# Optimization experiments

Measured on AMD Instinct MI355X. Metric: run time of the kernel, lower is better.

The kernel has to match this reference:

```python
import jax, jax.numpy as jnp
import numpy as np

NUM_HEADS = 16
NUM_KV_HEADS = 4
HEAD_DIM = 128
HALF_DIM = HEAD_DIM // 2
LAMBDA_INIT = 0.8
LAMBDA_MIN = 0.0
LAMBDA_MAX = 1.0
CAUSAL = True
NORMALIZE_DIFF = True
NEG = -1.0e9


def setup_inputs() -> dict:
    key = jax.random.key(0)
    k1, k2, k3 = jax.random.split(key, 3)
    B, Sq, Sk = 1, 2048, 2048
    query = jax.random.normal(k1, (B, NUM_HEADS, Sq, HEAD_DIM), dtype=jnp.float32)
    key_t = jax.random.normal(k2, (B, NUM_KV_HEADS, Sk, HEAD_DIM), dtype=jnp.float32)
    value = jax.random.normal(k3, (B, NUM_KV_HEADS, Sk, HEAD_DIM), dtype=jnp.float32)
    return {"query": query, "key": key_t, "value": value}


def reference(query, key, value):
    scale = 1.0 / (HALF_DIM ** 0.5)
    lam = jnp.clip(jnp.float32(LAMBDA_INIT), LAMBDA_MIN, LAMBDA_MAX)
    # GQA: repeat KV heads to match query heads
    rep = NUM_HEADS // NUM_KV_HEADS
    k = jnp.repeat(key, rep, axis=1)    # [b,h,k,d]
    v = jnp.repeat(value, rep, axis=1)  # [b,h,k,d]
    q1, q2 = query[..., :HALF_DIM], query[..., HALF_DIM:]
    k1, k2 = k[..., :HALF_DIM], k[..., HALF_DIM:]
    scores1 = jnp.einsum('bhqd,bhkd->bhqk', q1, k1) * scale
    scores2 = jnp.einsum('bhqd,bhkd->bhqk', q2, k2) * scale
    if CAUSAL:
        Sq, Sk = query.shape[2], k.shape[2]
        mask = jnp.tril(jnp.ones((Sq, Sk), dtype=jnp.float32))  # lower-triangular causal
        scores1 = scores1 * mask + (1.0 - mask) * NEG
        scores2 = scores2 * mask + (1.0 - mask) * NEG
    attn1 = jax.nn.softmax(scores1, axis=-1)
    attn2 = jax.nn.softmax(scores2, axis=-1)
    diff_attn = attn1 - lam * attn2
    out = jnp.einsum('bhqk,bhkd->bhqd', diff_attn, v)
    if NORMALIZE_DIFF:
        out = out * (1.0 - LAMBDA_INIT)
    return out
```

## Files before the change

kernel.cpp:

```cpp
#include <hip/hip_runtime.h>

#define NUM_HEADS 16
#define HEAD_DIM  128
#define SEQ       2048

typedef __attribute__((ext_vector_type(8))) unsigned short us8;
typedef __attribute__((ext_vector_type(8))) __bf16 bf16x8;
typedef __attribute__((ext_vector_type(4))) float f32x4;
typedef __attribute__((ext_vector_type(16))) float f32x16;
typedef __attribute__((ext_vector_type(4))) unsigned u32x4;

static __device__ inline unsigned short f2bf(float x) {
    union { float f; unsigned u; } v; v.f = x;
    unsigned r = v.u + 0x7FFFu + ((v.u >> 16) & 1u);
    return (unsigned short)(r >> 16);
}
static __device__ inline float bf2f(unsigned short h) {
    union { float f; unsigned u; } v; v.u = ((unsigned)h) << 16;
    return v.f;
}
static __device__ inline unsigned pk2bf(float a, float b) {
    return (unsigned)f2bf(a) | ((unsigned)f2bf(b) << 16);
}
static __device__ inline float fast_exp2(float x) {
#if __has_builtin(__builtin_amdgcn_exp2f)
    return __builtin_amdgcn_exp2f(x);
#else
    return exp2f(x);
#endif
}
static __device__ inline f32x16 mfma32(us8 a, us8 b, f32x16 c) {
    return __builtin_amdgcn_mfma_f32_32x32x16_bf16(
        __builtin_bit_cast(bf16x8, a), __builtin_bit_cast(bf16x8, b), c, 0, 0, 0);
}

__global__ __launch_bounds__(256)
void prep_kv(const float* __restrict__ K, const float* __restrict__ V,
             unsigned short* __restrict__ Kbf, unsigned short* __restrict__ Vtb)
{
    const int bx = (int)blockIdx.x, t = (int)threadIdx.x;
    __shared__ __align__(16) float Ls[64][130];
    if (bx < 512) {
        const size_t base = ((size_t)bx * 256 + t) * 8;
        float x[8];
        *(float4*)&x[0] = *(const float4*)(K + base);
        *(float4*)&x[4] = *(const float4*)(K + base + 4);
        u32x4 pk;
        #pragma unroll
        for (int j = 0; j < 4; ++j) pk[j] = pk2bf(x[2*j], x[2*j+1]);
        *(us8*)(Kbf + base) = __builtin_bit_cast(us8, pk);
    } else {
        const int b2 = bx - 512, kvh = b2 >> 5, tile = b2 & 31;
        const float* vb = V + ((size_t)kvh * SEQ + tile * 64) * HEAD_DIM;
        #pragma unroll
        for (int i = 0; i < 8; ++i) {
            const int idx = t + i * 256;
            const int r = idx >> 5, c4 = idx & 31;
            *(float4*)&Ls[r][c4 * 4] = *(const float4*)(vb + (size_t)r * HEAD_DIM + c4 * 4);
        }
        __syncthreads();
        const int d = t & 127, kh = t >> 7;
        unsigned pk[16];
        #pragma unroll
        for (int j = 0; j < 16; ++j)
            pk[j] = pk2bf(Ls[kh * 32 + 2*j][d], Ls[kh * 32 + 2*j + 1][d]);
        unsigned short* dst = Vtb + ((size_t)(kvh * 32 + tile) * 128 + d) * 64 + kh * 32;
        #pragma unroll
        for (int blk = 0; blk < 4; ++blk)
            *(us8*)(dst + blk * 8) = *(us8*)&pk[blk * 4];
    }
}

#define KB0 0
#define KB1 16384
#define VB0 32768
#define VB1 49152

__global__ __launch_bounds__(256, 2)
void diff_attn_mfma6(const float* __restrict__ Q,
                     const unsigned short* __restrict__ Kbf,
                     const unsigned short* __restrict__ Vtb,
                     float* __restrict__ Out)
{
    __shared__ __align__(16) unsigned char smem[65536];
    __shared__ float rsb[2][2][32];

    const int t   = (int)threadIdx.x;
    const int wv  = t >> 6;
    const int ln  = t & 63;
    const int mat = wv >> 1;
    const int kh  = wv & 1;
    const int q   = ln & 31;
    const int H   = ln >> 5;

    const int bx   = (int)blockIdx.x;
    const int h    = bx & 15;
    const int idx  = bx >> 4;
    const int qtA  = idx, qtB = 63 - idx;
    const int nktA = (qtA >> 1) + 1;
    const int kvh  = h >> 2;

    const unsigned short* Kt0 = Kbf + (size_t)kvh * SEQ * HEAD_DIM;
    const unsigned short* Vt0 = Vtb + (size_t)kvh * 32 * 128 * 64;

    const float qscale = 0.125f * 1.44269504088896340736f;

    us8 qhi[4], qlo[4];
    auto loadQ = [&](int q0c) {
        const float* qr = Q + ((size_t)h * SEQ + q0c + q) * HEAD_DIM + mat * 64;
        #pragma unroll
        for (int ds = 0; ds < 4; ++ds) {
            const int d0 = ds * 16 + H * 8;
            float x[8];
            *(float4*)&x[0] = *(const float4*)(qr + d0);
            *(float4*)&x[4] = *(const float4*)(qr + d0 + 4);
            us8 hi8, lo8;
            #pragma unroll
            for (int j = 0; j < 8; ++j) {
                float xs = x[j] * qscale;
                unsigned short hb = f2bf(xs);
                hi8[j] = hb;
                lo8[j] = f2bf(xs - bf2f(hb));
            }
            qhi[ds] = hi8; qlo[ds] = lo8;
        }
    };

    f32x16 o[4];
    f32x4 rsv;
    #pragma unroll
    for (int i = 0; i < 4; ++i) o[i] = (f32x16)0.f;
    rsv = (f32x4)0.f;

    auto issue = [&](int kt, int par) {
        unsigned char* kb = smem + (par ? KB1 : KB0);
        unsigned char* vb = smem + (par ? VB1 : VB0);
        #pragma unroll
        for (int i = 0; i < 4; ++i) {
            const int L = i * 256 + t;
            const int r = L >> 4, g = (L & 15) ^ (r & 15);
            const unsigned short* gp = Kt0 + (size_t)(kt * 64 + r) * 128 + g * 8;
            __builtin_amdgcn_global_load_lds(
                (const __attribute__((address_space(1))) unsigned*)gp,
                (__attribute__((address_space(3))) unsigned*)(kb + (size_t)(i * 256 + wv * 64) * 16),
                16, 0, 0);
        }
        #pragma unroll
        for (int i = 0; i < 4; ++i) {
            const int L = i * 256 + t;
            const int r = L >> 3, g = (L & 7) ^ (r & 7);
            const unsigned short* gp = Vt0 + (size_t)(kt * 128 + r) * 64 + g * 8;
            __builtin_amdgcn_global_load_lds(
                (const __attribute__((address_space(1))) unsigned*)gp,
                (__attribute__((address_space(3))) unsigned*)(vb + (size_t)(i * 256 + wv * 64) * 16),
                16, 0, 0);
        }
    };

    auto epilogue = [&](int q0c, int epar) {
        __syncthreads();
        float rsc = (rsv[0] + rsv[1]) + (rsv[2] + rsv[3]);
        rsc += __shfl_xor(rsc, 32, 64);
        if (ln < 32) rsb[mat][kh][ln] = rsc;
        float* cbK = (float*)(smem + (epar ? KB1 : KB0));
        float* cbV = (float*)(smem + (epar ? VB1 : VB0));
        float* cbM = mat ? cbV : cbK;
        if (kh == 1) {
            #pragma unroll
            for (int db = 0; db < 4; ++db)
                #pragma unroll
                for (int i = 0; i < 4; ++i) {
                    f32x4 v = { o[db][i*4+0], o[db][i*4+1], o[db][i*4+2], o[db][i*4+3] };
                    *(f32x4*)(cbM + q * 128 + ((((db<<3)+(i<<1)+H) ^ q) << 2)) = v;
                }
        }
        __syncthreads();
        if (kh == 0) {
            const float l = rsb[mat][0][q] + rsb[mat][1][q];
            const float a = mat ? (0.16f / l) : (0.2f / l);
            #pragma unroll
            for (int db = 0; db < 4; ++db)
                #pragma unroll
                for (int i = 0; i < 4; ++i) {
                    f32x4 v = *(f32x4*)(cbM + q * 128 + ((((db<<3)+(i<<1)+H) ^ q) << 2));
                    #pragma unroll
                    for (int jj = 0; jj < 4; ++jj)
                        o[db][i*4+jj] = (o[db][i*4+jj] + v[jj]) * a;
                }
            if (mat == 1) {
                #pragma unroll
                for (int db = 0; db < 4; ++db)
                    #pragma unroll
                    for (int i = 0; i < 4; ++i) {
                        f32x4 v = { o[db][i*4+0], o[db][i*4+1], o[db][i*4+2], o[db][i*4+3] };
                        *(f32x4*)(cbV + q * 128 + ((((db<<3)+(i<<1)+H) ^ q) << 2)) = v;
                    }
            }
        }
        __syncthreads();
        if (wv == 0) {
            float* ob = Out + ((size_t)h * SEQ + q0c + q) * HEAD_DIM;
            #pragma unroll
            for (int db = 0; db < 4; ++db)
                #pragma unroll
                for (int i = 0; i < 4; ++i) {
                    f32x4 v = *(f32x4*)(cbV + q * 128 + ((((db<<3)+(i<<1)+H) ^ q) << 2));
                    float4 r;
                    r.x = o[db][i*4+0] - v[0];
                    r.y = o[db][i*4+1] - v[1];
                    r.z = o[db][i*4+2] - v[2];
                    r.w = o[db][i*4+3] - v[3];
                    *(float4*)(ob + db * 32 + 8 * i + 4 * H) = r;
                }
        }
    };

    int q0 = qtA * 32, qt_cur = qtA;
    loadQ(q0);
    issue(0, 0);

    for (int j = 0; j < 33; ++j) {
        if (j == nktA) {
            epilogue(q0, (nktA - 1) & 1);
            q0 = qtB * 32; qt_cur = qtB;
            loadQ(q0);
            #pragma unroll
            for (int i = 0; i < 4; ++i) o[i] = (f32x16)0.f;
            rsv = (f32x4)0.f;
        }
        const int cur = j & 1;
        __syncthreads();
        if (j + 1 < 33) issue((j + 1 < nktA) ? j + 1 : j + 1 - nktA, cur ^ 1);

        const int kt = (j < nktA) ? j : j - nktA;
        const unsigned char* kbase = smem + (cur ? KB1 : KB0);
        const unsigned char* vbase = smem + (cur ? VB1 : VB0);
        const bool diag  = (j == nktA - 1) || (j == 32);
        const int  qpar  = qt_cur & 1;
        const bool skipw = diag && (qpar == 0) && (kh == 1);
        const bool triw  = diag && (kh == qpar);

        if (!skipw) {
            f32x16 s = (f32x16)0.f;
            const int krow = kh * 32 + q;
            #pragma unroll
            for (int ds = 0; ds < 4; ++ds) {
                us8 ak = *(const us8*)(kbase +
                          ((krow << 4) + ((mat * 8 + ds * 2 + H) ^ (krow & 15))) * 16);
                s = mfma32(ak, qhi[ds], s);
                s = mfma32(ak, qlo[ds], s);
            }
            unsigned c[16];
            if (triw) {
                const int kg0 = kt * 64 + kh * 32 + 4 * H;
                const int qg  = q0 + q;
                #pragma unroll
                for (int r = 0; r < 16; ++r) {
                    const int kg = kg0 + (r & 3) + ((r >> 2) << 3);
                    float e = (kg <= qg) ? fast_exp2(s[r]) : 0.f;
                    c[r] = __builtin_bit_cast(unsigned, e) & 0xffff0000u;
                    rsv[r & 3] += __builtin_bit_cast(float, c[r]);
                }
            } else {
                #pragma unroll
                for (int r = 0; r < 16; ++r) {
                    float e = fast_exp2(s[r]);
                    c[r] = __builtin_bit_cast(unsigned, e) & 0xffff0000u;
                    rsv[r & 3] += __builtin_bit_cast(float, c[r]);
                }
            }
            #pragma unroll
            for (int ks = 0; ks < 2; ++ks) {
                const unsigned pA = (c[8*ks+0] >> 16) | c[8*ks+1];
                const unsigned pB = (c[8*ks+2] >> 16) | c[8*ks+3];
                const unsigned pC = (c[8*ks+4] >> 16) | c[8*ks+5];
                const unsigned pD = (c[8*ks+6] >> 16) | c[8*ks+7];
                const unsigned x1 = H ? pA : pC;
                const unsigned x2 = H ? pB : pD;
                const unsigned t1 = (unsigned)__shfl_xor((int)x1, 32, 64);
                const unsigned t2 = (unsigned)__shfl_xor((int)x2, 32, 64);
                u32x4 bw;
                bw[0] = H ? t1 : pA;
                bw[1] = H ? t2 : pB;
                bw[2] = H ? pC : t1;
                bw[3] = H ? pD : t2;
                const us8 bp = __builtin_bit_cast(us8, bw);
                const int gb = kh * 4 + ks * 2 + H;
                #pragma unroll
                for (int db = 0; db < 4; ++db) {
                    const int r = db * 32 + q;
                    us8 av = *(const us8*)(vbase + ((r << 3) + (gb ^ (r & 7))) * 16);
                    o[db] = mfma32(av, bp, o[db]);
                }
            }
        }
    }

    epilogue(q0, 0);
}

extern "C" void kernel_launch(void* const* d_in, const int* in_sizes, int n_in,
                              void* d_out, int out_size, void* d_ws, size_t ws_size,
                              hipStream_t stream) {
    const float* Q = (const float*)d_in[0];
    const float* K = (const float*)d_in[1];
    const float* V = (const float*)d_in[2];
    float* Out = (float*)d_out;

    unsigned short* Kbf = (unsigned short*)d_ws;
    unsigned short* Vtb = Kbf + (size_t)4 * SEQ * HEAD_DIM;

    prep_kv<<<640, 256, 0, stream>>>(K, V, Kbf, Vtb);
    diff_attn_mfma6<<<512, 256, 0, stream>>>(Q, Kbf, Vtb, Out);
}
```

Before: 125.3 us.

## Pre-swizzle K/V into MFMA fragment layout and load directly to registers

The prep kernel now writes K and V in bf16 already arranged in per-lane MFMA operand fragment order. The attention kernel then loads each wave's operands straight from global memory into registers instead of staging tiles in LDS with global_load_lds and barriers. The next K tile is prefetched one iteration ahead in registers, and the per-iteration __syncthreads goes away. The cost is that each wave fetches its own fragments with no reuse through LDS, which relies on L2 and L1 caching and exposes more load latency. Register pressure also rises from holding 16 extra us8 fragments.

```diff
diff --git a/kernel.cpp b/kernel.cpp
--- a/kernel.cpp
+++ b/kernel.cpp
@@ -3,6 +3,7 @@
 #define NUM_HEADS 16
 #define HEAD_DIM  128
 #define SEQ       2048
+#define KT_STRIDE 8192
 
 typedef __attribute__((ext_vector_type(8))) unsigned short us8;
 typedef __attribute__((ext_vector_type(8))) __bf16 bf16x8;
@@ -35,54 +36,62 @@
 }
 
 __global__ __launch_bounds__(256)
-void prep_kv(const float* __restrict__ K, const float* __restrict__ V,
-             unsigned short* __restrict__ Kbf, unsigned short* __restrict__ Vtb)
+void prep_frag(const float* __restrict__ K, const float* __restrict__ V,
+               unsigned short* __restrict__ KF, unsigned short* __restrict__ VF)
 {
-    const int bx = (int)blockIdx.x, t = (int)threadIdx.x;
-    __shared__ __align__(16) float Ls[64][130];
-    if (bx < 512) {
-        const size_t base = ((size_t)bx * 256 + t) * 8;
-        float x[8];
-        *(float4*)&x[0] = *(const float4*)(K + base);
-        *(float4*)&x[4] = *(const float4*)(K + base + 4);
-        u32x4 pk;
+    const int bx  = (int)blockIdx.x, t = (int)threadIdx.x;
+    const int which = bx & 1, kt = (bx >> 1) & 31, kvh = bx >> 6;
+    __shared__ __align__(16) float Ls[64][132];
+
+    const float* src = (which ? V : K) + ((size_t)kvh * SEQ + kt * 64) * HEAD_DIM;
+    #pragma unroll
+    for (int i = 0; i < 8; ++i) {
+        const int idx = t + i * 256;
+        const int r = idx >> 5, c4 = idx & 31;
+        *(float4*)&Ls[r][c4 * 4] = *(const float4*)(src + (size_t)r * HEAD_DIM + c4 * 4);
+    }
+    __syncthreads();
+
+    if (!which) {
         #pragma unroll
-        for (int j = 0; j < 4; ++j) pk[j] = pk2bf(x[2*j], x[2*j+1]);
-        *(us8*)(Kbf + base) = __builtin_bit_cast(us8, pk);
+        for (int i = 0; i < 4; ++i) {
+            const int c = t + i * 256;
+            const int lane = c & 63, ds = (c >> 6) & 3, mat = (c >> 8) & 1, kh = c >> 9;
+            const int H = lane >> 5;
+            const int row = kh * 32 + (lane & 31);
+            const int dim = mat * 64 + ds * 16 + H * 8;
+            u32x4 pk;
+            #pragma unroll
+            for (int jj = 0; jj < 4; ++jj)
+                pk[jj] = pk2bf(Ls[row][dim + 2*jj], Ls[row][dim + 2*jj + 1]);
+            *(us8*)(KF + ((size_t)(kvh * 32 + kt) * 16 + kh * 8 + mat * 4 + ds) * 512 + lane * 8)
+                = __builtin_bit_cast(us8, pk);
+        }
     } else {
-        const int b2 = bx - 512, kvh = b2 >> 5, tile = b2 & 31;
-        const float* vb = V + ((size_t)kvh * SEQ + tile * 64) * HEAD_DIM;
         #pragma unroll
-        for (int i = 0; i < 8; ++i) {
-            const int idx = t + i * 256;
-            const int r = idx >> 5, c4 = idx & 31;
-            *(float4*)&Ls[r][c4 * 4] = *(const float4*)(vb + (size_t)r * HEAD_DIM + c4 * 4);
-        }
-        __syncthreads();
-        const int d = t & 127, kh = t >> 7;
-        unsigned pk[16];
-        #pragma unroll
-        for (int j = 0; j < 16; ++j)
-            pk[j] = pk2bf(Ls[kh * 32 + 2*j][d], Ls[kh * 32 + 2*j + 1][d]);
-        unsigned short* dst = Vtb + ((size_t)(kvh * 32 + tile) * 128 + d) * 64 + kh * 32;
-        #pragma unroll
-        for (int blk = 0; blk < 4; ++blk)
-            *(us8*)(dst + blk * 8) = *(us8*)&pk[blk * 4];
+        for (int i = 0; i < 4; ++i) {
+            const int c = t + i * 256;
+            const int lane = c & 63, db = (c >> 6) & 3, ks = (c >> 8) & 1, kh = c >> 9;
+            const int H = lane >> 5;
+            const int s0 = kh * 32 + ks * 16 + H * 8;
+            const int d  = db * 32 + (lane & 31);
+            u32x4 pk;
+            #pragma unroll
+            for (int jj = 0; jj < 4; ++jj)
+                pk[jj] = pk2bf(Ls[s0 + 2*jj][d], Ls[s0 + 2*jj + 1][d]);
+            *(us8*)(VF + ((size_t)(kvh * 32 + kt) * 16 + kh * 8 + ks * 4 + db) * 512 + lane * 8)
+                = __builtin_bit_cast(us8, pk);
+        }
     }
 }
 
-#define KB0 0
-#define KB1 16384
-#define VB0 32768
-#define VB1 49152
-
 __global__ __launch_bounds__(256, 2)
-void diff_attn_mfma6(const float* __restrict__ Q,
-                     const unsigned short* __restrict__ Kbf,
-                     const unsigned short* __restrict__ Vtb,
+void diff_attn_mfma7(const float* __restrict__ Q,
+                     const unsigned short* __restrict__ KF,
+                     const unsigned short* __restrict__ VF,
                      float* __restrict__ Out)
 {
-    __shared__ __align__(16) unsigned char smem[65536];
+    __shared__ float cb[2][32][136];
     __shared__ float rsb[2][2][32];
 
     const int t   = (int)threadIdx.x;
@@ -100,8 +109,8 @@
     const int nktA = (qtA >> 1) + 1;
     const int kvh  = h >> 2;
 
-    const unsigned short* Kt0 = Kbf + (size_t)kvh * SEQ * HEAD_DIM;
-    const unsigned short* Vt0 = Vtb + (size_t)kvh * 32 * 128 * 64;
+    const unsigned short* kfb = KF + ((size_t)kvh * 32 * 16 + kh * 8 + mat * 4) * 512 + ln * 8;
+    const unsigned short* vfb = VF + ((size_t)kvh * 32 * 16 + kh * 8) * 512 + ln * 8;
 
     const float qscale = 0.125f * 1.44269504088896340736f;
 
@@ -127,51 +136,22 @@
     };
 
     f32x16 o[4];
-    f32x4 rsv;
+    f32x4  rsv = (f32x4)0.f;
     #pragma unroll
     for (int i = 0; i < 4; ++i) o[i] = (f32x16)0.f;
-    rsv = (f32x4)0.f;
-
-    auto issue = [&](int kt, int par) {
-        unsigned char* kb = smem + (par ? KB1 : KB0);
-        unsigned char* vb = smem + (par ? VB1 : VB0);
-        #pragma unroll
-        for (int i = 0; i < 4; ++i) {
-            const int L = i * 256 + t;
-            const int r = L >> 4, g = (L & 15) ^ (r & 15);
-            const unsigned short* gp = Kt0 + (size_t)(kt * 64 + r) * 128 + g * 8;
-            __builtin_amdgcn_global_load_lds(
-                (const __attribute__((address_space(1))) unsigned*)gp,
-                (__attribute__((address_space(3))) unsigned*)(kb + (size_t)(i * 256 + wv * 64) * 16),
-                16, 0, 0);
-        }
-        #pragma unroll
-        for (int i = 0; i < 4; ++i) {
-            const int L = i * 256 + t;
-            const int r = L >> 3, g = (L & 7) ^ (r & 7);
-            const unsigned short* gp = Vt0 + (size_t)(kt * 128 + r) * 64 + g * 8;
-            __builtin_amdgcn_global_load_lds(
-                (const __attribute__((address_space(1))) unsigned*)gp,
-                (__attribute__((address_space(3))) unsigned*)(vb + (size_t)(i * 256 + wv * 64) * 16),
-                16, 0, 0);
-        }
-    };
-
-    auto epilogue = [&](int q0c, int epar) {
+
+    auto epilogue = [&](int q0c) {
         __syncthreads();
         float rsc = (rsv[0] + rsv[1]) + (rsv[2] + rsv[3]);
         rsc += __shfl_xor(rsc, 32, 64);
         if (ln < 32) rsb[mat][kh][ln] = rsc;
-        float* cbK = (float*)(smem + (epar ? KB1 : KB0));
-        float* cbV = (float*)(smem + (epar ? VB1 : VB0));
-        float* cbM = mat ? cbV : cbK;
         if (kh == 1) {
             #pragma unroll
             for (int db = 0; db < 4; ++db)
                 #pragma unroll
                 for (int i = 0; i < 4; ++i) {
-                    f32x4 v = { o[db][i*4+0], o[db][i*4+1], o[db][i*4+2], o[db][i*4+3] };
-                    *(f32x4*)(cbM + q * 128 + ((((db<<3)+(i<<1)+H) ^ q) << 2)) = v;
+                    float4 v = { o[db][i*4+0], o[db][i*4+1], o[db][i*4+2], o[db][i*4+3] };
+                    *(float4*)&cb[mat][q][db * 32 + 8 * i + 4 * H] = v;
                 }
         }
         __syncthreads();
@@ -182,18 +162,19 @@
             for (int db = 0; db < 4; ++db)
                 #pragma unroll
                 for (int i = 0; i < 4; ++i) {
-                    f32x4 v = *(f32x4*)(cbM + q * 128 + ((((db<<3)+(i<<1)+H) ^ q) << 2));
-                    #pragma unroll
-                    for (int jj = 0; jj < 4; ++jj)
-                        o[db][i*4+jj] = (o[db][i*4+jj] + v[jj]) * a;
+                    float4 v = *(float4*)&cb[mat][q][db * 32 + 8 * i + 4 * H];
+                    o[db][i*4+0] = (o[db][i*4+0] + v.x) * a;
+                    o[db][i*4+1] = (o[db][i*4+1] + v.y) * a;
+                    o[db][i*4+2] = (o[db][i*4+2] + v.z) * a;
+                    o[db][i*4+3] = (o[db][i*4+3] + v.w) * a;
                 }
             if (mat == 1) {
                 #pragma unroll
                 for (int db = 0; db < 4; ++db)
                     #pragma unroll
                     for (int i = 0; i < 4; ++i) {
-                        f32x4 v = { o[db][i*4+0], o[db][i*4+1], o[db][i*4+2], o[db][i*4+3] };
-                        *(f32x4*)(cbV + q * 128 + ((((db<<3)+(i<<1)+H) ^ q) << 2)) = v;
+                        float4 v = { o[db][i*4+0], o[db][i*4+1], o[db][i*4+2], o[db][i*4+3] };
+                        *(float4*)&cb[1][q][db * 32 + 8 * i + 4 * H] = v;
                     }
             }
         }
@@ -204,51 +185,57 @@
             for (int db = 0; db < 4; ++db)
                 #pragma unroll
                 for (int i = 0; i < 4; ++i) {
-                    f32x4 v = *(f32x4*)(cbV + q * 128 + ((((db<<3)+(i<<1)+H) ^ q) << 2));
+                    float4 v = *(float4*)&cb[1][q][db * 32 + 8 * i + 4 * H];
                     float4 r;
-                    r.x = o[db][i*4+0] - v[0];
-                    r.y = o[db][i*4+1] - v[1];
-                    r.z = o[db][i*4+2] - v[2];
-                    r.w = o[db][i*4+3] - v[3];
+                    r.x = o[db][i*4+0] - v.x;
+                    r.y = o[db][i*4+1] - v.y;
+                    r.z = o[db][i*4+2] - v.z;
+                    r.w = o[db][i*4+3] - v.w;
                     *(float4*)(ob + db * 32 + 8 * i + 4 * H) = r;
                 }
         }
     };
 
-    int q0 = qtA * 32, qt_cur = qtA;
+    int q0 = qtA * 32, qpar = qtA & 1;
     loadQ(q0);
-    issue(0, 0);
+
+    us8 ka[4], kan[4], va[8];
+    #pragma unroll
+    for (int ds = 0; ds < 4; ++ds) ka[ds] = *(const us8*)(kfb + ds * 512);
 
     for (int j = 0; j < 33; ++j) {
         if (j == nktA) {
-            epilogue(q0, (nktA - 1) & 1);
-            q0 = qtB * 32; qt_cur = qtB;
+            epilogue(q0);
+            q0 = qtB * 32; qpar = qtB & 1;
             loadQ(q0);
             #pragma unroll
             for (int i = 0; i < 4; ++i) o[i] = (f32x16)0.f;
             rsv = (f32x4)0.f;
         }
-        const int cur = j & 1;
-        __syncthreads();
-        if (j + 1 < 33) issue((j + 1 < nktA) ? j + 1 : j + 1 - nktA, cur ^ 1);
-
         const int kt = (j < nktA) ? j : j - nktA;
-        const unsigned char* kbase = smem + (cur ? KB1 : KB0);
-        const unsigned char* vbase = smem + (cur ? VB1 : VB0);
+
+        {
+            const unsigned short* vb = vfb + (size_t)kt * KT_STRIDE;
+            #pragma unroll
+            for (int c = 0; c < 8; ++c) va[c] = *(const us8*)(vb + c * 512);
+        }
+        if (j + 1 < 33) {
+            const int nk = (j + 1 >= nktA) ? (j + 1 - nktA) : (j + 1);
+            const unsigned short* kb = kfb + (size_t)nk * KT_STRIDE;
+            #pragma unroll
+            for (int ds = 0; ds < 4; ++ds) kan[ds] = *(const us8*)(kb + ds * 512);
+        }
+
         const bool diag  = (j == nktA - 1) || (j == 32);
-        const int  qpar  = qt_cur & 1;
         const bool skipw = diag && (qpar == 0) && (kh == 1);
         const bool triw  = diag && (kh == qpar);
 
         if (!skipw) {
             f32x16 s = (f32x16)0.f;
-            const int krow = kh * 32 + q;
             #pragma unroll
             for (int ds = 0; ds < 4; ++ds) {
-                us8 ak = *(const us8*)(kbase +
-                          ((krow << 4) + ((mat * 8 + ds * 2 + H) ^ (krow & 15))) * 16);
-                s = mfma32(ak, qhi[ds], s);
-                s = mfma32(ak, qlo[ds], s);
+                s = mfma32(ka[ds], qhi[ds], s);
+                s = mfma32(ka[ds], qlo[ds], s);
             }
             unsigned c[16];
             if (triw) {
@@ -285,18 +272,17 @@
                 bw[2] = H ? pC : t1;
                 bw[3] = H ? pD : t2;
                 const us8 bp = __builtin_bit_cast(us8, bw);
-                const int gb = kh * 4 + ks * 2 + H;
-                #pragma unroll
-                for (int db = 0; db < 4; ++db) {
-                    const int r = db * 32 + q;
-                    us8 av = *(const us8*)(vbase + ((r << 3) + (gb ^ (r & 7))) * 16);
-                    o[db] = mfma32(av, bp, o[db]);
-                }
-            }
-        }
+                #pragma unroll
+                for (int db = 0; db < 4; ++db)
+                    o[db] = mfma32(va[ks * 4 + db], bp, o[db]);
+            }
+        }
+
+        #pragma unroll
+        for (int ds = 0; ds < 4; ++ds) ka[ds] = kan[ds];
     }
 
-    epilogue(q0, 0);
+    epilogue(q0);
 }
 
 extern "C" void kernel_launch(void* const* d_in, const int* in_sizes, int n_in,
@@ -307,9 +293,9 @@
     const float* V = (const float*)d_in[2];
     float* Out = (float*)d_out;
 
-    unsigned short* Kbf = (unsigned short*)d_ws;
-    unsigned short* Vtb = Kbf + (size_t)4 * SEQ * HEAD_DIM;
-
-    prep_kv<<<640, 256, 0, stream>>>(K, V, Kbf, Vtb);
-    diff_attn_mfma6<<<512, 256, 0, stream>>>(Q, Kbf, Vtb, Out);
-}
+    unsigned short* KF = (unsigned short*)d_ws;
+    unsigned short* VF = KF + (size_t)4 * SEQ * HEAD_DIM;
+
+    prep_frag<<<256, 256, 0, stream>>>(K, V, KF, VF);
+    diff_attn_mfma7<<<512, 256, 0, stream>>>(Q, KF, VF, Out);
+}
```

Measured after the change: 116.8 us. 6.9% less time.
